# Kernel tuning notes

Hardware: AMD Instinct MI355X
Metric: run time of the kernel (lower is better)

Reference implementation:

```python
import jax, jax.numpy as jnp
import numpy as np

NUM_FEATURES = 512
NUM_HID = 16
NUM_CLASSES = 40


def _glorot(key, shape):
    lim = float(np.sqrt(6.0 / (shape[0] + shape[1])))
    return jax.random.uniform(key, shape, jnp.float32, -lim, lim)


def setup_inputs() -> dict:
    key = jax.random.key(0)
    k1, k2, k3, k4 = jax.random.split(key, 4)
    N, E = 100000, 3200000
    x = jax.random.normal(k1, (N, NUM_FEATURES), jnp.float32)
    edge_index = jax.random.randint(k2, (2, E), 0, N, jnp.int64)
    W1 = _glorot(k3, (NUM_FEATURES, NUM_HID))
    b1 = jnp.zeros((NUM_HID,), jnp.float32)
    W2 = _glorot(k4, (NUM_HID, NUM_CLASSES))
    b2 = jnp.zeros((NUM_CLASSES,), jnp.float32)
    return {"x": x, "edge_index": edge_index, "num_nodes": N,
            "W1": W1, "b1": b1, "W2": W2, "b2": b2}


def gcn_conv(x, src, dst, norm, W, b, num_nodes):
    # linear transform first (PyG GCNConv), then normalized scatter-add
    h = x @ W                                    # [N, out]
    msg = h[src] * norm[:, None]                 # [E+N, out]
    agg = jax.ops.segment_sum(msg, dst, num_segments=num_nodes)
    return agg + b


def reference(x, edge_index, num_nodes, W1, b1, W2, b2):
    # add self-loops and compute symmetric normalization deg^-1/2 A_hat deg^-1/2
    loops = jnp.arange(num_nodes, dtype=edge_index.dtype)
    src = jnp.concatenate([edge_index[0], loops])
    dst = jnp.concatenate([edge_index[1], loops])
    ones = jnp.ones(src.shape, x.dtype)
    deg = jax.ops.segment_sum(ones, dst, num_segments=num_nodes)
    dinv = jnp.where(deg > 0, deg ** -0.5, 0.0)
    norm = dinv[src] * dinv[dst]

    h = jax.nn.relu(gcn_conv(x, src, dst, norm, W1, b1, num_nodes))
    # dropout omitted: inference mode (training=False)
    h = gcn_conv(h, src, dst, norm, W2, b2, num_nodes)
    out = jax.nn.softmax(h, axis=1)
    return (out, h)
```

## Files before the change

kernel.cpp:

```cpp
#include <hip/hip_runtime.h>
#include <math.h>

#define F 512
#define H 16
#define C 40
#define BW 128
#define BSH 7
#define NB_MAX 1024
#define CHUNK 4096
#define SRC_BITS 17
#define SRC_MASK 0x1FFFF
#define SORT_CAP 8192

__global__ void k_bhist(const int* __restrict__ dst, int* __restrict__ gbh,
                        int E, int NB) {
    __shared__ int hist[NB_MAX];
    for (int i = threadIdx.x; i < NB; i += 256) hist[i] = 0;
    __syncthreads();
    int c0 = blockIdx.x * CHUNK;
    int end = min(c0 + CHUNK, E);
    for (int i = c0 + threadIdx.x; i < end; i += 256)
        atomicAdd(&hist[dst[i] >> BSH], 1);
    __syncthreads();
    for (int i = threadIdx.x; i < NB; i += 256)
        if (hist[i]) atomicAdd(&gbh[i], hist[i]);
}

__global__ void k_bscan(const int* __restrict__ gbh, int* __restrict__ brow,
                        int* __restrict__ bcur, int* __restrict__ rowptr,
                        int NB, int N, int E) {
    __shared__ int s[1024];
    int t = threadIdx.x;
    int v = (t < NB) ? gbh[t] : 0;
    s[t] = v;
    __syncthreads();
    for (int off = 1; off < 1024; off <<= 1) {
        int add = (t >= off) ? s[t - off] : 0;
        __syncthreads();
        s[t] += add;
        __syncthreads();
    }
    if (t < NB) { int excl = s[t] - v; brow[t] = excl; bcur[t] = excl; }
    if (t == 0) { brow[NB] = E; rowptr[N] = E; }
}

__global__ void k_bscatter(const int* __restrict__ src, const int* __restrict__ dst,
                           int* __restrict__ bcur, int* __restrict__ ebuf,
                           int E, int NB) {
    __shared__ int lhist[NB_MAX];
    __shared__ int lbase[NB_MAX];
    __shared__ int lcur[NB_MAX];
    int c0 = blockIdx.x * CHUNK;
    int end = min(c0 + CHUNK, E);
    for (int i = threadIdx.x; i < NB; i += 256) lhist[i] = 0;
    __syncthreads();
    for (int i = c0 + threadIdx.x; i < end; i += 256)
        atomicAdd(&lhist[dst[i] >> BSH], 1);
    __syncthreads();
    for (int i = threadIdx.x; i < NB; i += 256) {
        int h = lhist[i];
        lbase[i] = h ? atomicAdd(&bcur[i], h) : 0;
        lcur[i] = 0;
    }
    __syncthreads();
    for (int i = c0 + threadIdx.x; i < end; i += 256) {
        int d = dst[i], sv = src[i];
        int b = d >> BSH;
        int r = atomicAdd(&lcur[b], 1);
        ebuf[lbase[b] + r] = ((d & (BW - 1)) << SRC_BITS) | sv;
    }
}

__global__ void k_sortb(int* __restrict__ ebuf, const int* __restrict__ brow,
                        int* __restrict__ rowptr, float* __restrict__ dinv, int N) {
    __shared__ int buf[SORT_CAP];
    __shared__ int hist[BW];
    __shared__ int off[BW];
    __shared__ int cur[BW];
    int b = blockIdx.x;
    int beg = brow[b], end = brow[b + 1];
    int len = end - beg;
    if (len > SORT_CAP) len = SORT_CAP;
    int tid = threadIdx.x;
    if (tid < BW) hist[tid] = 0;
    for (int i = tid; i < len; i += 256) buf[i] = ebuf[beg + i];
    __syncthreads();
    for (int i = tid; i < len; i += 256)
        atomicAdd(&hist[buf[i] >> SRC_BITS], 1);
    __syncthreads();
    if (tid < BW) off[tid] = hist[tid];
    __syncthreads();
    for (int d = 1; d < BW; d <<= 1) {
        int v = (tid < BW && tid >= d) ? off[tid - d] : 0;
        __syncthreads();
        if (tid < BW) off[tid] += v;
        __syncthreads();
    }
    if (tid < BW) {
        int excl = off[tid] - hist[tid];
        int n = b * BW + tid;
        if (n < N) {
            rowptr[n] = beg + excl;
            dinv[n] = rsqrtf((float)(hist[tid] + 1));
        }
        cur[tid] = excl;
    }
    __syncthreads();
    for (int i = tid; i < len; i += 256) {
        int w = buf[i];
        int r = atomicAdd(&cur[w >> SRC_BITS], 1);
        ebuf[beg + r] = w & SRC_MASK;
    }
}

__global__ void k_gemm1(const float* __restrict__ x, const float* __restrict__ W1,
                        const float* __restrict__ dinv, float* __restrict__ h0s, int N) {
    int v = blockIdx.x * 256 + threadIdx.x;
    if (v >= N) return;
    const float4* xr = (const float4*)(x + (size_t)v * F);
    float acc[H];
    #pragma unroll
    for (int j = 0; j < H; j++) acc[j] = 0.f;
    for (int k4 = 0; k4 < F / 4; k4++) {
        float4 xv = xr[k4];
        const float* w = W1 + k4 * 4 * H;
        #pragma unroll
        for (int j = 0; j < H; j++) acc[j] = fmaf(xv.x, w[j], acc[j]);
        #pragma unroll
        for (int j = 0; j < H; j++) acc[j] = fmaf(xv.y, w[H + j], acc[j]);
        #pragma unroll
        for (int j = 0; j < H; j++) acc[j] = fmaf(xv.z, w[2 * H + j], acc[j]);
        #pragma unroll
        for (int j = 0; j < H; j++) acc[j] = fmaf(xv.w, w[3 * H + j], acc[j]);
    }
    float dv = dinv[v];
    float4* o4 = (float4*)(h0s + (size_t)v * H);
    o4[0] = make_float4(acc[0] * dv, acc[1] * dv, acc[2] * dv, acc[3] * dv);
    o4[1] = make_float4(acc[4] * dv, acc[5] * dv, acc[6] * dv, acc[7] * dv);
    o4[2] = make_float4(acc[8] * dv, acc[9] * dv, acc[10] * dv, acc[11] * dv);
    o4[3] = make_float4(acc[12] * dv, acc[13] * dv, acc[14] * dv, acc[15] * dv);
}

__global__ void k_agg(const float* __restrict__ hs, const int* __restrict__ adj,
                      const int* __restrict__ rowptr, const float* __restrict__ dinv,
                      const float* __restrict__ b1, float* __restrict__ out,
                      int N, int relu_mode) {
    int t = blockIdx.x * 256 + threadIdx.x;
    int n = t >> 2, q = t & 3;
    if (n >= N) return;
    const float4* hs4 = (const float4*)hs;
    int beg = rowptr[n], end = rowptr[n + 1];
    float4 a = hs4[(size_t)n * 4 + q];
    float ax = a.x, ay = a.y, az = a.z, aw = a.w;
    int e = beg;
    for (; e + 3 < end; e += 4) {
        int s0 = adj[e], s1 = adj[e + 1], s2 = adj[e + 2], s3 = adj[e + 3];
        float4 v0 = hs4[(size_t)s0 * 4 + q];
        float4 v1 = hs4[(size_t)s1 * 4 + q];
        float4 v2 = hs4[(size_t)s2 * 4 + q];
        float4 v3 = hs4[(size_t)s3 * 4 + q];
        ax += (v0.x + v1.x) + (v2.x + v3.x);
        ay += (v0.y + v1.y) + (v2.y + v3.y);
        az += (v0.z + v1.z) + (v2.z + v3.z);
        aw += (v0.w + v1.w) + (v2.w + v3.w);
    }
    for (; e < end; e++) {
        int s = adj[e];
        float4 v = hs4[(size_t)s * 4 + q];
        ax += v.x; ay += v.y; az += v.z; aw += v.w;
    }
    float dv = dinv[n];
    float4 r;
    if (relu_mode) {
        r.x = fmaxf(fmaf(dv, ax, b1[q * 4 + 0]), 0.f) * dv;
        r.y = fmaxf(fmaf(dv, ay, b1[q * 4 + 1]), 0.f) * dv;
        r.z = fmaxf(fmaf(dv, az, b1[q * 4 + 2]), 0.f) * dv;
        r.w = fmaxf(fmaf(dv, aw, b1[q * 4 + 3]), 0.f) * dv;
    } else {
        r.x = dv * ax; r.y = dv * ay; r.z = dv * az; r.w = dv * aw;
    }
    ((float4*)out)[(size_t)n * 4 + q] = r;
}

__global__ void k_out(const float* __restrict__ g2, const float* __restrict__ W2,
                      const float* __restrict__ b2, float* __restrict__ dout, int N) {
    int t = blockIdx.x * 256 + threadIdx.x;
    int n = t >> 6, lane = t & 63;
    if (n >= N) return;
    const float* g = g2 + (size_t)n * H;
    float acc = 0.f;
    #pragma unroll
    for (int k = 0; k < H; k++) {
        float w = (lane < C) ? W2[k * C + lane] : 0.f;
        acc = fmaf(g[k], w, acc);
    }
    float h2 = (lane < C) ? acc + b2[lane] : -INFINITY;
    float m = h2;
    #pragma unroll
    for (int off = 32; off; off >>= 1) m = fmaxf(m, __shfl_xor(m, off, 64));
    float ex = (lane < C) ? __expf(h2 - m) : 0.f;
    float s = ex;
    #pragma unroll
    for (int off = 32; off; off >>= 1) s += __shfl_xor(s, off, 64);
    if (lane < C) {
        float inv = 1.f / s;
        dout[(size_t)n * C + lane] = ex * inv;
        dout[(size_t)N * C + (size_t)n * C + lane] = h2;
    }
}

extern "C" void kernel_launch(void* const* d_in, const int* in_sizes, int n_in,
                              void* d_out, int out_size, void* d_ws, size_t ws_size,
                              hipStream_t stream) {
    const float* x  = (const float*)d_in[0];
    const int*   ei = (const int*)d_in[1];
    const float* W1 = (const float*)d_in[3];
    const float* b1 = (const float*)d_in[4];
    const float* W2 = (const float*)d_in[5];
    const float* b2 = (const float*)d_in[6];
    float* out = (float*)d_out;

    int N = in_sizes[0] / F;
    int E = in_sizes[1] / 2;
    const int* src = ei;
    const int* dst = ei + E;
    int NB = (N + BW - 1) / BW;

    float* ws = (float*)d_ws;
    size_t o = 0;
    int* gbh    = (int*)(ws + o); o += (size_t)NB_MAX;
    int* brow   = (int*)(ws + o); o += (size_t)NB_MAX + 4;
    int* bcur   = (int*)(ws + o); o += (size_t)NB_MAX;
    int* rowptr = (int*)(ws + o); o += (size_t)N + 4;
    int* ebuf   = (int*)(ws + o); o += (size_t)E;
    float* dinv = ws + o;         o += (size_t)N;
    float* h0s  = ws + o;         o += (size_t)N * H;
    float* h1s  = ws + o;         o += (size_t)N * H;
    float* g2   = ws + o;         o += (size_t)N * H;

    int nb  = (N + 255) / 256;
    int nch = (E + CHUNK - 1) / CHUNK;

    hipMemsetAsync(gbh, 0, (size_t)NB_MAX * sizeof(int), stream);
    k_bhist   <<<nch, 256, 0, stream>>>(dst, gbh, E, NB);
    k_bscan   <<<1, 1024, 0, stream>>>(gbh, brow, bcur, rowptr, NB, N, E);
    k_bscatter<<<nch, 256, 0, stream>>>(src, dst, bcur, ebuf, E, NB);
    k_sortb   <<<NB, 256, 0, stream>>>(ebuf, brow, rowptr, dinv, N);
    k_gemm1   <<<nb, 256, 0, stream>>>(x, W1, dinv, h0s, N);
    k_agg     <<<(N * 4 + 255) / 256, 256, 0, stream>>>(h0s, ebuf, rowptr, dinv, b1, h1s, N, 1);
    k_agg     <<<(N * 4 + 255) / 256, 256, 0, stream>>>(h1s, ebuf, rowptr, dinv, b1, g2, N, 0);
    k_out     <<<(N * 64 + 255) / 256, 256, 0, stream>>>(g2, W2, b2, out, N);
}
```

Before: 630.3 us.

## Coalesce bucket scatter via shared-memory local sort and stage GEMM1 x tiles in LDS

The bucket scatter kernel now reads each chunk once into shared memory, builds a local bucket-sorted permutation, and writes edges to global memory in bucket-contiguous order. This replaces the second pass over dst and the random per-edge writes. The first GEMM now stages 256x32 tiles of x through padded LDS so that global loads are coalesced across the row-per-thread layout. Launch bounds are added to all kernels. The cost is more LDS per block, which may lower occupancy, plus extra barriers.

```diff
diff --git a/kernel.cpp b/kernel.cpp
--- a/kernel.cpp
+++ b/kernel.cpp
@@ -8,12 +8,13 @@
 #define BSH 7
 #define NB_MAX 1024
 #define CHUNK 4096
+#define SCH 4096
 #define SRC_BITS 17
 #define SRC_MASK 0x1FFFF
 #define SORT_CAP 8192
 
-__global__ void k_bhist(const int* __restrict__ dst, int* __restrict__ gbh,
-                        int E, int NB) {
+__global__ __launch_bounds__(256) void k_bhist(const int* __restrict__ dst,
+                                               int* __restrict__ gbh, int E, int NB) {
     __shared__ int hist[NB_MAX];
     for (int i = threadIdx.x; i < NB; i += 256) hist[i] = 0;
     __syncthreads();
@@ -44,35 +45,72 @@
     if (t == 0) { brow[NB] = E; rowptr[N] = E; }
 }
 
-__global__ void k_bscatter(const int* __restrict__ src, const int* __restrict__ dst,
-                           int* __restrict__ bcur, int* __restrict__ ebuf,
-                           int E, int NB) {
-    __shared__ int lhist[NB_MAX];
-    __shared__ int lbase[NB_MAX];
-    __shared__ int lcur[NB_MAX];
-    int c0 = blockIdx.x * CHUNK;
-    int end = min(c0 + CHUNK, E);
-    for (int i = threadIdx.x; i < NB; i += 256) lhist[i] = 0;
-    __syncthreads();
-    for (int i = c0 + threadIdx.x; i < end; i += 256)
-        atomicAdd(&lhist[dst[i] >> BSH], 1);
-    __syncthreads();
-    for (int i = threadIdx.x; i < NB; i += 256) {
-        int h = lhist[i];
-        lbase[i] = h ? atomicAdd(&bcur[i], h) : 0;
-        lcur[i] = 0;
-    }
-    __syncthreads();
-    for (int i = c0 + threadIdx.x; i < end; i += 256) {
-        int d = dst[i], sv = src[i];
+__global__ __launch_bounds__(256) void k_bscatter(const int* __restrict__ src,
+                                                  const int* __restrict__ dst,
+                                                  int* __restrict__ bcur,
+                                                  int* __restrict__ ebuf, int E, int NB) {
+    __shared__ int            spk[SCH];
+    __shared__ unsigned short sb[SCH];
+    __shared__ int            inv[SCH];
+    __shared__ int            hist[NB_MAX];
+    __shared__ int            loff[NB_MAX];
+    __shared__ int            gbase[NB_MAX];
+    __shared__ int            wsum[4];
+    int t = threadIdx.x;
+    int c0 = blockIdx.x * SCH;
+    int len = min(c0 + SCH, E) - c0;
+    for (int i = t; i < NB_MAX; i += 256) hist[i] = 0;
+    __syncthreads();
+    for (int i = t; i < len; i += 256) {
+        int d = dst[c0 + i], sv = src[c0 + i];
         int b = d >> BSH;
-        int r = atomicAdd(&lcur[b], 1);
-        ebuf[lbase[b] + r] = ((d & (BW - 1)) << SRC_BITS) | sv;
-    }
-}
-
-__global__ void k_sortb(int* __restrict__ ebuf, const int* __restrict__ brow,
-                        int* __restrict__ rowptr, float* __restrict__ dinv, int N) {
+        spk[i] = ((d & (BW - 1)) << SRC_BITS) | sv;
+        sb[i] = (unsigned short)b;
+        atomicAdd(&hist[b], 1);
+    }
+    __syncthreads();
+    int b0 = t * 4;
+    int h0 = hist[b0], h1 = hist[b0 + 1], h2 = hist[b0 + 2], h3 = hist[b0 + 3];
+    int s = h0 + h1 + h2 + h3;
+    int lane = t & 63, wv = t >> 6;
+    int inc = s;
+    #pragma unroll
+    for (int off = 1; off < 64; off <<= 1) {
+        int u = __shfl_up(inc, off, 64);
+        if (lane >= off) inc += u;
+    }
+    if (lane == 63) wsum[wv] = inc;
+    __syncthreads();
+    int wof = 0;
+    for (int w = 0; w < wv; w++) wof += wsum[w];
+    int excl = wof + inc - s;
+    loff[b0]     = excl;
+    loff[b0 + 1] = excl + h0;
+    loff[b0 + 2] = excl + h0 + h1;
+    loff[b0 + 3] = excl + h0 + h1 + h2;
+    gbase[b0]     = h0 ? atomicAdd(&bcur[b0],     h0) : 0;
+    gbase[b0 + 1] = h1 ? atomicAdd(&bcur[b0 + 1], h1) : 0;
+    gbase[b0 + 2] = h2 ? atomicAdd(&bcur[b0 + 2], h2) : 0;
+    gbase[b0 + 3] = h3 ? atomicAdd(&bcur[b0 + 3], h3) : 0;
+    hist[b0] = 0; hist[b0 + 1] = 0; hist[b0 + 2] = 0; hist[b0 + 3] = 0;
+    __syncthreads();
+    for (int i = t; i < len; i += 256) {
+        int b = sb[i];
+        int r = atomicAdd(&hist[b], 1);
+        inv[loff[b] + r] = i;
+    }
+    __syncthreads();
+    for (int p = t; p < len; p += 256) {
+        int j = inv[p];
+        int b = sb[j];
+        ebuf[gbase[b] + (p - loff[b])] = spk[j];
+    }
+}
+
+__global__ __launch_bounds__(256) void k_sortb(int* __restrict__ ebuf,
+                                               const int* __restrict__ brow,
+                                               int* __restrict__ rowptr,
+                                               float* __restrict__ dinv, int N) {
     __shared__ int buf[SORT_CAP];
     __shared__ int hist[BW];
     __shared__ int off[BW];
@@ -113,26 +151,41 @@
     }
 }
 
-__global__ void k_gemm1(const float* __restrict__ x, const float* __restrict__ W1,
-                        const float* __restrict__ dinv, float* __restrict__ h0s, int N) {
-    int v = blockIdx.x * 256 + threadIdx.x;
+#define KT 32
+__global__ __launch_bounds__(256) void k_gemm1(const float* __restrict__ x,
+                                               const float* __restrict__ W1,
+                                               const float* __restrict__ dinv,
+                                               float* __restrict__ h0s, int N) {
+    __shared__ float xs[256 * 33];
+    int t = threadIdx.x;
+    int v0 = blockIdx.x * 256;
+    float acc[H];
+    #pragma unroll
+    for (int j = 0; j < H; j++) acc[j] = 0.f;
+    for (int kt = 0; kt < F; kt += KT) {
+        __syncthreads();
+        #pragma unroll
+        for (int p = 0; p < 8; p++) {
+            int idx = t + p * 256;
+            int row = idx >> 3, c4 = idx & 7;
+            int v = v0 + row;
+            float4 val = (v < N) ? *(const float4*)(x + (size_t)v * F + kt + c4 * 4)
+                                 : make_float4(0.f, 0.f, 0.f, 0.f);
+            float* dp = &xs[row * 33 + c4 * 4];
+            dp[0] = val.x; dp[1] = val.y; dp[2] = val.z; dp[3] = val.w;
+        }
+        __syncthreads();
+        const float* xr = &xs[t * 33];
+        #pragma unroll
+        for (int k = 0; k < KT; k++) {
+            float xv = xr[k];
+            const float* w = W1 + (size_t)(kt + k) * H;
+            #pragma unroll
+            for (int j = 0; j < H; j++) acc[j] = fmaf(xv, w[j], acc[j]);
+        }
+    }
+    int v = v0 + t;
     if (v >= N) return;
-    const float4* xr = (const float4*)(x + (size_t)v * F);
-    float acc[H];
-    #pragma unroll
-    for (int j = 0; j < H; j++) acc[j] = 0.f;
-    for (int k4 = 0; k4 < F / 4; k4++) {
-        float4 xv = xr[k4];
-        const float* w = W1 + k4 * 4 * H;
-        #pragma unroll
-        for (int j = 0; j < H; j++) acc[j] = fmaf(xv.x, w[j], acc[j]);
-        #pragma unroll
-        for (int j = 0; j < H; j++) acc[j] = fmaf(xv.y, w[H + j], acc[j]);
-        #pragma unroll
-        for (int j = 0; j < H; j++) acc[j] = fmaf(xv.z, w[2 * H + j], acc[j]);
-        #pragma unroll
-        for (int j = 0; j < H; j++) acc[j] = fmaf(xv.w, w[3 * H + j], acc[j]);
-    }
     float dv = dinv[v];
     float4* o4 = (float4*)(h0s + (size_t)v * H);
     o4[0] = make_float4(acc[0] * dv, acc[1] * dv, acc[2] * dv, acc[3] * dv);
@@ -141,10 +194,13 @@
     o4[3] = make_float4(acc[12] * dv, acc[13] * dv, acc[14] * dv, acc[15] * dv);
 }
 
-__global__ void k_agg(const float* __restrict__ hs, const int* __restrict__ adj,
-                      const int* __restrict__ rowptr, const float* __restrict__ dinv,
-                      const float* __restrict__ b1, float* __restrict__ out,
-                      int N, int relu_mode) {
+__global__ __launch_bounds__(256) void k_agg(const float* __restrict__ hs,
+                                             const int* __restrict__ adj,
+                                             const int* __restrict__ rowptr,
+                                             const float* __restrict__ dinv,
+                                             const float* __restrict__ b1,
+                                             float* __restrict__ out,
+                                             int N, int relu_mode) {
     int t = blockIdx.x * 256 + threadIdx.x;
     int n = t >> 2, q = t & 3;
     if (n >= N) return;
@@ -182,8 +238,10 @@
     ((float4*)out)[(size_t)n * 4 + q] = r;
 }
 
-__global__ void k_out(const float* __restrict__ g2, const float* __restrict__ W2,
-                      const float* __restrict__ b2, float* __restrict__ dout, int N) {
+__global__ __launch_bounds__(256) void k_out(const float* __restrict__ g2,
+                                             const float* __restrict__ W2,
+                                             const float* __restrict__ b2,
+                                             float* __restrict__ dout, int N) {
     int t = blockIdx.x * 256 + threadIdx.x;
     int n = t >> 6, lane = t & 63;
     if (n >= N) return;
@@ -240,11 +298,12 @@
 
     int nb  = (N + 255) / 256;
     int nch = (E + CHUNK - 1) / CHUNK;
+    int nsc = (E + SCH - 1) / SCH;
 
     hipMemsetAsync(gbh, 0, (size_t)NB_MAX * sizeof(int), stream);
     k_bhist   <<<nch, 256, 0, stream>>>(dst, gbh, E, NB);
     k_bscan   <<<1, 1024, 0, stream>>>(gbh, brow, bcur, rowptr, NB, N, E);
-    k_bscatter<<<nch, 256, 0, stream>>>(src, dst, bcur, ebuf, E, NB);
+    k_bscatter<<<nsc, 256, 0, stream>>>(src, dst, bcur, ebuf, E, NB);
     k_sortb   <<<NB, 256, 0, stream>>>(ebuf, brow, rowptr, dinv, N);
     k_gemm1   <<<nb, 256, 0, stream>>>(x, W1, dinv, h0s, N);
     k_agg     <<<(N * 4 + 255) / 256, 256, 0, stream>>>(h0s, ebuf, rowptr, dinv, b1, h1s, N, 1);
```

Result: slower. 669.7 us (+6.3%).
